# Kernel optimization log

Hardware: AMD Instinct MI355X
Metric: run time of the kernel (lower is better)

## Reference

```python
import jax, jax.numpy as jnp
import numpy as np

B, T, N, C = 8, 16, 2048, 512


def setup_inputs() -> dict:
    key = jax.random.key(0)
    k1, k2, k3, k4, k5, k6 = jax.random.split(key, 6)
    return {
        "vd_s": jax.random.normal(k1, (B, T, C), dtype=jnp.float32),
        "vd_nodes": jax.random.normal(k2, (B, N, C), dtype=jnp.float32),
        # 1x1 conv weights initialized N(0, 0.01) as in the torch module
        "W1": jax.random.normal(k3, (C, C), dtype=jnp.float32) * 0.01,
        "b1": jax.random.normal(k4, (C,), dtype=jnp.float32) * 0.01,
        "W2": jax.random.normal(k5, (C, C), dtype=jnp.float32) * 0.01,
        "b2": jax.random.normal(k6, (C,), dtype=jnp.float32) * 0.01,
    }


def reference(vd_s, vd_nodes, W1, b1, W2, b2):
    # propagation_step = 1 (as in the original module)
    def per_graph(s, nodes):
        # s: [T, C] scene features, nodes: [N, C] node features
        out_scene = s.mean(axis=0)                     # [C]
        state = nodes                                  # [N, C]
        # 1x1 convs on [N, C, 1, 1] == per-node linear layers
        mat1 = state @ W1.T + b1                       # [N, C]
        mat2 = state @ W2.T + b2                       # [N, C]
        adj = mat1 @ mat2.T                            # [N, N]
        soft_adj = jax.nn.softmax(adj, axis=1)         # row-softmax (dim=1)
        new_state = soft_adj @ state + state           # message update + residual
        gp_out = new_state.mean(axis=0)                # [C]
        return jnp.concatenate([out_scene, gp_out], axis=0)  # [2C]

    return jax.vmap(per_graph)(vd_s, vd_nodes)         # [B, 2C]
```

## Files before the change

kernel.cpp:

```cpp
#include <hip/hip_runtime.h>

typedef __bf16 bf16;
typedef __bf16 bf16x8 __attribute__((ext_vector_type(8), aligned(16)));
typedef float  f32x4  __attribute__((ext_vector_type(4)));

#define B_ 8
#define T_ 16
#define N_ 2048
#define C_ 512

__device__ inline bf16x8 load8_f32(const float* p) {
    float4 a = *(const float4*)p;
    float4 b = *(const float4*)(p + 4);
    bf16x8 r;
    r[0] = (bf16)a.x; r[1] = (bf16)a.y; r[2] = (bf16)a.z; r[3] = (bf16)a.w;
    r[4] = (bf16)b.x; r[5] = (bf16)b.y; r[6] = (bf16)b.z; r[7] = (bf16)b.w;
    return r;
}

__device__ inline void gload_lds16(const bf16* g, bf16* l) {
    __builtin_amdgcn_global_load_lds(
        (const __attribute__((address_space(1))) void*)g,
        (__attribute__((address_space(3))) void*)l, 16, 0, 0);
}

__global__ __launch_bounds__(256) void k_prep(
    const float* __restrict__ vd_s, const float* __restrict__ nodes,
    const float* __restrict__ W1, const float* __restrict__ W2,
    float* __restrict__ out, bf16* __restrict__ nodes_bf,
    bf16* __restrict__ W1t, bf16* __restrict__ W2t) {
    __shared__ float sh[32 * 33];
    const int bx = blockIdx.x, tid = threadIdx.x;
    if (bx < 2048) {
        size_t i = ((size_t)bx * 256 + tid) * 16;
        *(bf16x8*)(nodes_bf + i)     = load8_f32(nodes + i);
        *(bf16x8*)(nodes_bf + i + 8) = load8_f32(nodes + i + 8);
    } else if (bx < 2064) {
        int gt = (bx - 2048) * 256 + tid;
        int b = gt >> 9, c = gt & 511;
        float s = 0.f;
#pragma unroll
        for (int t = 0; t < T_; ++t) s += vd_s[(size_t)b * T_ * C_ + t * C_ + c];
        out[b * 2 * C_ + c] = s * (1.0f / T_);
    } else {
        const float* W = (bx < 2320) ? W1 : W2;
        bf16* Wt = (bx < 2320) ? W1t : W2t;
        int idx = (bx < 2320) ? bx - 2064 : bx - 2320;
        int bxx = (idx & 15) * 32, byy = (idx >> 4) * 32;
        int tx = tid & 31, ty = tid >> 5;
#pragma unroll
        for (int r = 0; r < 32; r += 8)
            sh[(ty + r) * 33 + tx] = W[(size_t)(byy + ty + r) * C_ + bxx + tx];
        __syncthreads();
#pragma unroll
        for (int r = 0; r < 32; r += 8)
            Wt[(size_t)(bxx + ty + r) * C_ + byy + tx] = (bf16)sh[tx * 33 + ty + r];
    }
}

__global__ void k_q(const float* __restrict__ b1, const bf16* __restrict__ W2t,
                    float* __restrict__ q) {
    int wid = threadIdx.x >> 6, lane = threadIdx.x & 63;
    int c = blockIdx.x * 4 + wid;
    bf16x8 v8 = *(const bf16x8*)(W2t + (size_t)c * C_ + lane * 8);
    float s = 0.f;
#pragma unroll
    for (int i = 0; i < 8; ++i) s += (float)v8[i] * b1[lane * 8 + i];
#pragma unroll
    for (int m = 32; m; m >>= 1) s += __shfl_xor(s, m);
    if (lane == 0) q[c] = s;
}

__global__ __launch_bounds__(256) void gemm_nt(
    const bf16* __restrict__ A, size_t strideA,
    const bf16* __restrict__ Bm, size_t strideB,
    const float* __restrict__ bias,
    bf16* __restrict__ C, size_t strideC,
    int N, int K) {
    __shared__ __attribute__((aligned(16))) bf16 lA[128 * 64];
    __shared__ __attribute__((aligned(16))) bf16 lB[128 * 64];
    const int tid = threadIdx.x;
    const int lane = tid & 63, w = tid >> 6;
    const int wm = w >> 1, wn = w & 1;
    const int z = blockIdx.z;
    const int bm = blockIdx.x * 128, bn = blockIdx.y * 128;
    const bf16* Ab = A + (size_t)z * strideA;
    const bf16* Bb = Bm + (size_t)z * strideB;

    f32x4 acc[4][4];
#pragma unroll
    for (int i = 0; i < 4; ++i)
#pragma unroll
        for (int j = 0; j < 4; ++j) acc[i][j] = f32x4{0.f, 0.f, 0.f, 0.f};

    const int nkt = K >> 6;
    for (int kt = 0; kt < nkt; ++kt) {
#pragma unroll
        for (int c = 0; c < 4; ++c) {
            int ca = c * 256 + tid;
            int row = ca >> 3;
            int qd = (ca & 7) ^ (row & 7);
            gload_lds16(Ab + (size_t)(bm + row) * K + kt * 64 + qd * 8,
                        lA + c * 2048 + w * 512);
            gload_lds16(Bb + (size_t)(bn + row) * K + kt * 64 + qd * 8,
                        lB + c * 2048 + w * 512);
        }
        __syncthreads();

        bf16x8 af[2][4], bfr[2][4];
#pragma unroll
        for (int ks = 0; ks < 2; ++ks) {
            int y = ks * 4 + (lane >> 4);
#pragma unroll
            for (int i = 0; i < 4; ++i) {
                int ra = wm * 64 + i * 16 + (lane & 15);
                int rb = wn * 64 + i * 16 + (lane & 15);
                af[ks][i]  = *(const bf16x8*)&lA[ra * 64 + ((y ^ (ra & 7)) * 8)];
                bfr[ks][i] = *(const bf16x8*)&lB[rb * 64 + ((y ^ (rb & 7)) * 8)];
            }
        }
#pragma unroll
        for (int ks = 0; ks < 2; ++ks)
#pragma unroll
            for (int i = 0; i < 4; ++i)
#pragma unroll
                for (int j = 0; j < 4; ++j)
                    acc[i][j] = __builtin_amdgcn_mfma_f32_16x16x32_bf16(
                        af[ks][i], bfr[ks][j], acc[i][j], 0, 0, 0);
        __syncthreads();
    }

    bf16* Cb = C + (size_t)z * strideC;
#pragma unroll
    for (int i = 0; i < 4; ++i) {
#pragma unroll
        for (int j = 0; j < 4; ++j) {
            int col = bn + wn * 64 + j * 16 + (lane & 15);
            float bv = bias ? bias[col] : 0.f;
#pragma unroll
            for (int r = 0; r < 4; ++r) {
                int row = bm + wm * 64 + i * 16 + (lane >> 4) * 4 + r;
                Cb[(size_t)row * N + col] = (bf16)(acc[i][j][r] + bv);
            }
        }
    }
}

__global__ __launch_bounds__(512, 2) void gemm256p(
    const bf16* __restrict__ A, const bf16* __restrict__ Bm,
    bf16* __restrict__ P) {
    __shared__ __attribute__((aligned(16))) bf16 ls[2][2][16384];
    const int tid = threadIdx.x;
    const int lane = tid & 63, w = tid >> 6;
    const int wm = w >> 2, wn = w & 3;
    const int id = blockIdx.x;
    const int sw = (id & 7) * 64 + (id >> 3);
    const int z = sw >> 6, tt = sw & 63;
    const int bm = (tt >> 3) * 256, bn = (tt & 7) * 256;
    const bf16* Ab = A + (size_t)z * N_ * C_;
    const bf16* Bb = Bm + (size_t)z * N_ * C_;

    f32x4 acc[8][4];
#pragma unroll
    for (int i = 0; i < 8; ++i)
#pragma unroll
        for (int j = 0; j < 4; ++j) acc[i][j] = f32x4{0.f, 0.f, 0.f, 0.f};

#define STAGE_H(MATP, BASE, h, kt_, buf_, abi)                                    \
    {                                                                             \
        _Pragma("unroll")                                                         \
        for (int sl = 0; sl < 2; ++sl) {                                          \
            int cc = sl * 512 + tid;                                              \
            int row = (h) * 128 + (cc >> 3);                                      \
            int qd = (cc & 7) ^ (row & 7);                                        \
            gload_lds16(MATP + (size_t)((BASE) + row) * C_ + (kt_) * 64 + qd * 8, \
                        &ls[buf_][abi][((h) * 1024 + sl * 512 + w * 64) * 8]);    \
        }                                                                         \
    }
#define PH_SYNC_MFMA                                                    \
    __builtin_amdgcn_s_barrier();                                       \
    asm volatile("s_waitcnt lgkmcnt(0)" ::: "memory");                  \
    __builtin_amdgcn_sched_barrier(0);                                  \
    __builtin_amdgcn_s_setprio(1);

    STAGE_H(Ab, bm, 0, 0, 0, 0); STAGE_H(Ab, bm, 1, 0, 0, 0);
    STAGE_H(Bb, bn, 0, 0, 0, 1); STAGE_H(Bb, bn, 1, 0, 0, 1);
    STAGE_H(Bb, bn, 0, 1, 1, 1); STAGE_H(Bb, bn, 1, 1, 1, 1);
    asm volatile("s_waitcnt vmcnt(4)" ::: "memory");
    __builtin_amdgcn_s_barrier();

#pragma unroll
    for (int j = 0; j < 8; ++j) {
        const int cur = j & 1, nxt = cur ^ 1;
        const bf16* lA = &ls[cur][0][0];
        const bf16* lB = &ls[cur][1][0];
        bf16x8 af[4][2], b0[2][2], b1v[2][2];

#pragma unroll
        for (int i = 0; i < 4; ++i) {
            int ra = wm * 128 + i * 16 + (lane & 15);
#pragma unroll
            for (int ks = 0; ks < 2; ++ks) {
                int y = ks * 4 + (lane >> 4);
                af[i][ks] = *(const bf16x8*)&lA[ra * 64 + ((y ^ (ra & 7)) * 8)];
            }
        }
#pragma unroll
        for (int jj = 0; jj < 2; ++jj) {
            int rb = wn * 64 + jj * 16 + (lane & 15);
#pragma unroll
            for (int ks = 0; ks < 2; ++ks) {
                int y = ks * 4 + (lane >> 4);
                b0[jj][ks] = *(const bf16x8*)&lB[rb * 64 + ((y ^ (rb & 7)) * 8)];
            }
        }
        if (j < 7) STAGE_H(Ab, bm, 0, j + 1, nxt, 0);
        PH_SYNC_MFMA
#pragma unroll
        for (int ks = 0; ks < 2; ++ks)
#pragma unroll
            for (int i = 0; i < 4; ++i)
#pragma unroll
                for (int jj = 0; jj < 2; ++jj)
                    acc[i][jj] = __builtin_amdgcn_mfma_f32_16x16x32_bf16(
                        af[i][ks], b0[jj][ks], acc[i][jj], 0, 0, 0);
        __builtin_amdgcn_s_setprio(0);
        __builtin_amdgcn_s_barrier();

#pragma unroll
        for (int jj = 0; jj < 2; ++jj) {
            int rb = wn * 64 + 32 + jj * 16 + (lane & 15);
#pragma unroll
            for (int ks = 0; ks < 2; ++ks) {
                int y = ks * 4 + (lane >> 4);
                b1v[jj][ks] = *(const bf16x8*)&lB[rb * 64 + ((y ^ (rb & 7)) * 8)];
            }
        }
        if (j < 7) STAGE_H(Ab, bm, 1, j + 1, nxt, 0);
        PH_SYNC_MFMA
#pragma unroll
        for (int ks = 0; ks < 2; ++ks)
#pragma unroll
            for (int i = 0; i < 4; ++i)
#pragma unroll
                for (int jj = 0; jj < 2; ++jj)
                    acc[i][2 + jj] = __builtin_amdgcn_mfma_f32_16x16x32_bf16(
                        af[i][ks], b1v[jj][ks], acc[i][2 + jj], 0, 0, 0);
        __builtin_amdgcn_s_setprio(0);
        __builtin_amdgcn_s_barrier();

#pragma unroll
        for (int i = 0; i < 4; ++i) {
            int ra = wm * 128 + 64 + i * 16 + (lane & 15);
#pragma unroll
            for (int ks = 0; ks < 2; ++ks) {
                int y = ks * 4 + (lane >> 4);
                af[i][ks] = *(const bf16x8*)&lA[ra * 64 + ((y ^ (ra & 7)) * 8)];
            }
        }
        if (j < 6) STAGE_H(Bb, bn, 0, j + 2, cur, 1);
        PH_SYNC_MFMA
#pragma unroll
        for (int ks = 0; ks < 2; ++ks)
#pragma unroll
            for (int i = 0; i < 4; ++i)
#pragma unroll
                for (int jj = 0; jj < 2; ++jj)
                    acc[4 + i][jj] = __builtin_amdgcn_mfma_f32_16x16x32_bf16(
                        af[i][ks], b0[jj][ks], acc[4 + i][jj], 0, 0, 0);
        __builtin_amdgcn_s_setprio(0);
        __builtin_amdgcn_s_barrier();

        if (j < 6) {
            STAGE_H(Bb, bn, 1, j + 2, cur, 1);
            asm volatile("s_waitcnt vmcnt(4)" ::: "memory");
        } else if (j == 6) {
            asm volatile("s_waitcnt vmcnt(0)" ::: "memory");
        }
        __builtin_amdgcn_s_barrier();
        __builtin_amdgcn_s_setprio(1);
#pragma unroll
        for (int ks = 0; ks < 2; ++ks)
#pragma unroll
            for (int i = 0; i < 4; ++i)
#pragma unroll
                for (int jj = 0; jj < 2; ++jj)
                    acc[4 + i][2 + jj] = __builtin_amdgcn_mfma_f32_16x16x32_bf16(
                        af[i][ks], b1v[jj][ks], acc[4 + i][2 + jj], 0, 0, 0);
        __builtin_amdgcn_s_setprio(0);
        __builtin_amdgcn_s_barrier();
    }

    bf16* Pb = P + (size_t)z * N_ * N_;
#pragma unroll
    for (int fi = 0; fi < 8; ++fi) {
#pragma unroll
        for (int fj = 0; fj < 4; ++fj) {
            int roff = (fi >> 2) * 64 + (fi & 3) * 16;
            int coff = (fj >> 1) * 32 + (fj & 1) * 16;
            int col = bn + wn * 64 + coff + (lane & 15);
#pragma unroll
            for (int r = 0; r < 4; ++r) {
                int row = bm + wm * 128 + roff + (lane >> 4) * 4 + r;
                float v = __expf(fminf(acc[fi][fj][r], 30.f));
                Pb[(size_t)row * N_ + col] = (bf16)v;
            }
        }
    }
#undef STAGE_H
#undef PH_SYNC_MFMA
}

__global__ __launch_bounds__(256) void k_w2(const bf16* __restrict__ P,
                                            float* __restrict__ wpart) {
    __shared__ float rp[16 * 256];
    __shared__ float ri[16];
    const int tid = threadIdx.x;
    const int s = blockIdx.x, b = blockIdx.y;
    const bf16* Pb = P + (size_t)b * N_ * N_ + (size_t)s * 16 * N_;
    const int j0 = tid * 8;
    bf16x8 v[16];
#pragma unroll
    for (int r = 0; r < 16; ++r) {
        v[r] = *(const bf16x8*)&Pb[(size_t)r * N_ + j0];
        float t = 0.f;
#pragma unroll
        for (int e = 0; e < 8; ++e) t += (float)v[r][e];
        rp[r * 256 + tid] = t;
    }
    __syncthreads();
    {
        int row = tid >> 4, seg = tid & 15;
        float t = 0.f;
#pragma unroll
        for (int k = 0; k < 16; ++k) t += rp[row * 256 + seg + 16 * k];
#pragma unroll
        for (int m = 8; m; m >>= 1) t += __shfl_xor(t, m);
        if (seg == 0) ri[row] = 1.0f / t;
    }
    __syncthreads();
    float acc8[8] = {0.f, 0.f, 0.f, 0.f, 0.f, 0.f, 0.f, 0.f};
#pragma unroll
    for (int r = 0; r < 16; ++r) {
        float rr = ri[r];
#pragma unroll
        for (int e = 0; e < 8; ++e) acc8[e] += rr * (float)v[r][e];
    }
    float* wp = wpart + ((size_t)b * 128 + s) * (size_t)N_;
#pragma unroll
    for (int e = 0; e < 8; ++e) wp[j0 + e] = acc8[e];
}

__global__ __launch_bounds__(256) void k_gp(const bf16* __restrict__ nodes_bf,
                                            const float* __restrict__ wpart,
                                            float* __restrict__ gppart) {
    __shared__ float wred[4][64];
    __shared__ float wsh[64];
    __shared__ float gred[4][512];
    const int tid = threadIdx.x;
    const int slab = blockIdx.x, b = blockIdx.y;
    const int jj = tid & 63, sg = tid >> 6;
    float wacc = 0.f;
    for (int s = sg; s < 128; s += 4)
        wacc += wpart[((size_t)b * 128 + s) * N_ + slab * 64 + jj];
    wred[sg][jj] = wacc;
    __syncthreads();
    if (tid < 64)
        wsh[tid] = wred[0][tid] + wred[1][tid] + wred[2][tid] + wred[3][tid] + 1.0f;
    __syncthreads();
    const int j0 = slab * 64;
    const int cc = (tid & 63) * 8, jr = tid >> 6;
    const bf16* nb = nodes_bf + (size_t)b * N_ * C_;
    float acc8[8] = {0.f, 0.f, 0.f, 0.f, 0.f, 0.f, 0.f, 0.f};
    for (int j = jr; j < 64; j += 4) {
        float wj = wsh[j];
        bf16x8 nv = *(const bf16x8*)&nb[(size_t)(j0 + j) * C_ + cc];
#pragma unroll
        for (int e = 0; e < 8; ++e) acc8[e] += wj * (float)nv[e];
    }
#pragma unroll
    for (int e = 0; e < 8; ++e) gred[jr][cc + e] = acc8[e];
    __syncthreads();
    if (tid < 64) {
#pragma unroll
        for (int e = 0; e < 8; ++e) {
            int c = tid * 8 + e;
            gppart[((size_t)slab * 8 + b) * C_ + c] =
                gred[0][c] + gred[1][c] + gred[2][c] + gred[3][c];
        }
    }
}

__global__ void k_fin(const float* __restrict__ gppart, float* __restrict__ out) {
    int gt = blockIdx.x * 256 + threadIdx.x;
    int b = gt >> 9, c = gt & 511;
    float s = 0.f;
#pragma unroll
    for (int k = 0; k < 32; ++k) s += gppart[((size_t)k * 8 + b) * C_ + c];
    out[b * 2 * C_ + C_ + c] = s * (1.0f / N_);
}

extern "C" void kernel_launch(void* const* d_in, const int* in_sizes, int n_in,
                              void* d_out, int out_size, void* d_ws, size_t ws_size,
                              hipStream_t stream) {
    const float* vd_s  = (const float*)d_in[0];
    const float* nodes = (const float*)d_in[1];
    const float* W1    = (const float*)d_in[2];
    const float* b1    = (const float*)d_in[3];
    const float* W2    = (const float*)d_in[4];
    float* out = (float*)d_out;

    char* ws = (char*)d_ws;
    bf16*  nodes_bf = (bf16*)(ws);
    bf16*  H2       = (bf16*)(ws + ((size_t)16 << 20));
    float* wpart    = (float*)(ws + ((size_t)16 << 20));
    bf16*  P        = (bf16*)(ws + ((size_t)32 << 20));
    bf16*  W1t      = (bf16*)(ws + ((size_t)96 << 20));
    bf16*  W2t      = (bf16*)(ws + ((size_t)96 << 20) + (512u << 10));
    bf16*  Gt       = (bf16*)(ws + ((size_t)96 << 20) + (1024u << 10));
    char*  fbase    = ws + ((size_t)96 << 20) + (1536u << 10);
    float* q        = (float*)(fbase);
    float* gppart   = (float*)(fbase + 4096);

    k_prep<<<2576, 256, 0, stream>>>(vd_s, nodes, W1, W2,
                                     out, nodes_bf, W1t, W2t);
    k_q<<<128, 256, 0, stream>>>(b1, W2t, q);

    gemm_nt<<<dim3(4, 4, 1), 256, 0, stream>>>(
        W2t, 0, W1t, 0, nullptr, Gt, 0, C_, C_);
    gemm_nt<<<dim3(16, 4, 8), 256, 0, stream>>>(
        nodes_bf, (size_t)N_ * C_, Gt, 0, q,
        H2, (size_t)N_ * C_, C_, C_);
    gemm256p<<<512, 512, 0, stream>>>(H2, nodes_bf, P);

    k_w2<<<dim3(128, 8), 256, 0, stream>>>(P, wpart);
    k_gp<<<dim3(32, 8), 256, 0, stream>>>(nodes_bf, wpart, gppart);
    k_fin<<<16, 256, 0, stream>>>(gppart, out);
}
```

Before: 115.4 us.

## Software-pipeline LDS fragment reads across MFMA phases in adj GEMM

```diff
diff --git a/kernel.cpp b/kernel.cpp
--- a/kernel.cpp
+++ b/kernel.cpp
@@ -177,99 +177,89 @@
                         &ls[buf_][abi][((h) * 1024 + sl * 512 + w * 64) * 8]);    \
         }                                                                         \
     }
-#define PH_SYNC_MFMA                                                    \
-    __builtin_amdgcn_s_barrier();                                       \
-    asm volatile("s_waitcnt lgkmcnt(0)" ::: "memory");                  \
-    __builtin_amdgcn_sched_barrier(0);                                  \
-    __builtin_amdgcn_s_setprio(1);
+#define READ_A(LAp, HALF)                                                         \
+    {                                                                             \
+        _Pragma("unroll")                                                         \
+        for (int i = 0; i < 4; ++i) {                                             \
+            int ra = wm * 128 + (HALF) * 64 + i * 16 + (lane & 15);               \
+            _Pragma("unroll")                                                     \
+            for (int ks = 0; ks < 2; ++ks) {                                      \
+                int y = ks * 4 + (lane >> 4);                                     \
+                af[i][ks] = *(const bf16x8*)&(LAp)[ra * 64 + ((y ^ (ra & 7)) * 8)]; \
+            }                                                                     \
+        }                                                                         \
+    }
+#define READ_B(BDST, LBp, HOFF)                                                   \
+    {                                                                             \
+        _Pragma("unroll")                                                         \
+        for (int jj = 0; jj < 2; ++jj) {                                          \
+            int rb = wn * 64 + (HOFF) + jj * 16 + (lane & 15);                    \
+            _Pragma("unroll")                                                     \
+            for (int ks = 0; ks < 2; ++ks) {                                      \
+                int y = ks * 4 + (lane >> 4);                                     \
+                BDST[jj][ks] = *(const bf16x8*)&(LBp)[rb * 64 + ((y ^ (rb & 7)) * 8)]; \
+            }                                                                     \
+        }                                                                         \
+    }
+#define MFMA8(AROW, BCOL, BSRC)                                                   \
+    {                                                                             \
+        _Pragma("unroll")                                                         \
+        for (int ks = 0; ks < 2; ++ks)                                            \
+            _Pragma("unroll")                                                     \
+            for (int i = 0; i < 4; ++i)                                           \
+                _Pragma("unroll")                                                 \
+                for (int jj = 0; jj < 2; ++jj)                                    \
+                    acc[(AROW) + i][(BCOL) + jj] =                                \
+                        __builtin_amdgcn_mfma_f32_16x16x32_bf16(                  \
+                            af[i][ks], BSRC[jj][ks],                              \
+                            acc[(AROW) + i][(BCOL) + jj], 0, 0, 0);               \
+    }
+
+    bf16x8 af[4][2], b0[2][2], b1v[2][2];
 
     STAGE_H(Ab, bm, 0, 0, 0, 0); STAGE_H(Ab, bm, 1, 0, 0, 0);
     STAGE_H(Bb, bn, 0, 0, 0, 1); STAGE_H(Bb, bn, 1, 0, 0, 1);
     STAGE_H(Bb, bn, 0, 1, 1, 1); STAGE_H(Bb, bn, 1, 1, 1, 1);
     asm volatile("s_waitcnt vmcnt(4)" ::: "memory");
     __builtin_amdgcn_s_barrier();
+    READ_B(b0, (&ls[0][1][0]), 0)
+    READ_A((&ls[0][0][0]), 0)
+    __builtin_amdgcn_sched_barrier(0);
 
 #pragma unroll
     for (int j = 0; j < 8; ++j) {
         const int cur = j & 1, nxt = cur ^ 1;
-        const bf16* lA = &ls[cur][0][0];
-        const bf16* lB = &ls[cur][1][0];
-        bf16x8 af[4][2], b0[2][2], b1v[2][2];
-
-#pragma unroll
-        for (int i = 0; i < 4; ++i) {
-            int ra = wm * 128 + i * 16 + (lane & 15);
-#pragma unroll
-            for (int ks = 0; ks < 2; ++ks) {
-                int y = ks * 4 + (lane >> 4);
-                af[i][ks] = *(const bf16x8*)&lA[ra * 64 + ((y ^ (ra & 7)) * 8)];
-            }
-        }
-#pragma unroll
-        for (int jj = 0; jj < 2; ++jj) {
-            int rb = wn * 64 + jj * 16 + (lane & 15);
-#pragma unroll
-            for (int ks = 0; ks < 2; ++ks) {
-                int y = ks * 4 + (lane >> 4);
-                b0[jj][ks] = *(const bf16x8*)&lB[rb * 64 + ((y ^ (rb & 7)) * 8)];
-            }
-        }
+        const bf16* lA  = &ls[cur][0][0];
+        const bf16* lB  = &ls[cur][1][0];
+        const bf16* lAn = &ls[nxt][0][0];
+        const bf16* lBn = &ls[nxt][1][0];
+
+        __builtin_amdgcn_s_barrier();
+        READ_B(b1v, lB, 32)
         if (j < 7) STAGE_H(Ab, bm, 0, j + 1, nxt, 0);
-        PH_SYNC_MFMA
-#pragma unroll
-        for (int ks = 0; ks < 2; ++ks)
-#pragma unroll
-            for (int i = 0; i < 4; ++i)
-#pragma unroll
-                for (int jj = 0; jj < 2; ++jj)
-                    acc[i][jj] = __builtin_amdgcn_mfma_f32_16x16x32_bf16(
-                        af[i][ks], b0[jj][ks], acc[i][jj], 0, 0, 0);
+        asm volatile("s_waitcnt lgkmcnt(4)" ::: "memory");
+        __builtin_amdgcn_sched_barrier(0);
+        __builtin_amdgcn_s_setprio(1);
+        MFMA8(0, 0, b0)
         __builtin_amdgcn_s_setprio(0);
+
         __builtin_amdgcn_s_barrier();
-
-#pragma unroll
-        for (int jj = 0; jj < 2; ++jj) {
-            int rb = wn * 64 + 32 + jj * 16 + (lane & 15);
-#pragma unroll
-            for (int ks = 0; ks < 2; ++ks) {
-                int y = ks * 4 + (lane >> 4);
-                b1v[jj][ks] = *(const bf16x8*)&lB[rb * 64 + ((y ^ (rb & 7)) * 8)];
-            }
-        }
         if (j < 7) STAGE_H(Ab, bm, 1, j + 1, nxt, 0);
-        PH_SYNC_MFMA
-#pragma unroll
-        for (int ks = 0; ks < 2; ++ks)
-#pragma unroll
-            for (int i = 0; i < 4; ++i)
-#pragma unroll
-                for (int jj = 0; jj < 2; ++jj)
-                    acc[i][2 + jj] = __builtin_amdgcn_mfma_f32_16x16x32_bf16(
-                        af[i][ks], b1v[jj][ks], acc[i][2 + jj], 0, 0, 0);
+        asm volatile("s_waitcnt lgkmcnt(0)" ::: "memory");
+        __builtin_amdgcn_sched_barrier(0);
+        __builtin_amdgcn_s_setprio(1);
+        MFMA8(0, 2, b1v)
         __builtin_amdgcn_s_setprio(0);
+        READ_A(lA, 1)
+        __builtin_amdgcn_sched_barrier(0);
+
         __builtin_amdgcn_s_barrier();
-
-#pragma unroll
-        for (int i = 0; i < 4; ++i) {
-            int ra = wm * 128 + 64 + i * 16 + (lane & 15);
-#pragma unroll
-            for (int ks = 0; ks < 2; ++ks) {
-                int y = ks * 4 + (lane >> 4);
-                af[i][ks] = *(const bf16x8*)&lA[ra * 64 + ((y ^ (ra & 7)) * 8)];
-            }
-        }
         if (j < 6) STAGE_H(Bb, bn, 0, j + 2, cur, 1);
-        PH_SYNC_MFMA
-#pragma unroll
-        for (int ks = 0; ks < 2; ++ks)
-#pragma unroll
-            for (int i = 0; i < 4; ++i)
-#pragma unroll
-                for (int jj = 0; jj < 2; ++jj)
-                    acc[4 + i][jj] = __builtin_amdgcn_mfma_f32_16x16x32_bf16(
-                        af[i][ks], b0[jj][ks], acc[4 + i][jj], 0, 0, 0);
+        asm volatile("s_waitcnt lgkmcnt(0)" ::: "memory");
+        __builtin_amdgcn_sched_barrier(0);
+        __builtin_amdgcn_s_setprio(1);
+        MFMA8(4, 0, b0)
         __builtin_amdgcn_s_setprio(0);
-        __builtin_amdgcn_s_barrier();
 
         if (j < 6) {
             STAGE_H(Bb, bn, 1, j + 2, cur, 1);
@@ -278,17 +268,13 @@
             asm volatile("s_waitcnt vmcnt(0)" ::: "memory");
         }
         __builtin_amdgcn_s_barrier();
+        if (j < 7) READ_B(b0, lBn, 0)
+        __builtin_amdgcn_sched_barrier(0);
         __builtin_amdgcn_s_setprio(1);
-#pragma unroll
-        for (int ks = 0; ks < 2; ++ks)
-#pragma unroll
-            for (int i = 0; i < 4; ++i)
-#pragma unroll
-                for (int jj = 0; jj < 2; ++jj)
-                    acc[4 + i][2 + jj] = __builtin_amdgcn_mfma_f32_16x16x32_bf16(
-                        af[i][ks], b1v[jj][ks], acc[4 + i][2 + jj], 0, 0, 0);
+        MFMA8(4, 2, b1v)
         __builtin_amdgcn_s_setprio(0);
-        __builtin_amdgcn_s_barrier();
+        if (j < 7) READ_A(lAn, 0)
+        __builtin_amdgcn_sched_barrier(0);
     }
 
     bf16* Pb = P + (size_t)z * N_ * N_;
@@ -308,7 +294,9 @@
         }
     }
 #undef STAGE_H
-#undef PH_SYNC_MFMA
+#undef READ_A
+#undef READ_B
+#undef MFMA8
 }
 
 __global__ __launch_bounds__(256) void k_w2(const bf16* __restrict__ P,
```

Measured after the change: 115.5 us. Within noise of the previous version (+0.1%).
